# Optimization experiments

Hardware: AMD Instinct MI355X
Metric: run time of the kernel (lower is better)

## Reference

```python
import jax, jax.numpy as jnp
import numpy as np

N = 300000   # number of occupied voxels (sparse tensor rows)
L = 100      # grid side length -> 1e6 cells, occupancy 0.3
C = 32       # channels (channelwise/depthwise conv)
KS = 3       # kernel_size per axis
D = 3        # spatial dimension
R = (KS - 1) // 2


def _build_sparse_structure():
    """Sample N unique voxel coords and build kernel maps (edge lists) like
    MinkowskiEngine's coordinate manager: for each kernel offset, pairs
    (in_idx, out_idx) such that coords[in_idx] == coords[out_idx] + offset."""
    rng = np.random.default_rng(0)
    flat = rng.choice(L ** 3, size=N, replace=False)
    coords = np.stack([flat // (L * L), (flat // L) % L, flat % L], axis=1).astype(np.int32)
    keys = flat.astype(np.int64)
    order = np.argsort(keys)
    sk = keys[order]
    out_ids = np.arange(N, dtype=np.int64)
    in_list, out_list = [], []
    for dx in range(-R, R + 1):
        for dy in range(-R, R + 1):
            for dz in range(-R, R + 1):
                nx = coords[:, 0].astype(np.int64) + dx
                ny = coords[:, 1].astype(np.int64) + dy
                nz = coords[:, 2].astype(np.int64) + dz
                inb = (nx >= 0) & (nx < L) & (ny >= 0) & (ny < L) & (nz >= 0) & (nz < L)
                nk = (nx * L + ny) * L + nz
                pos = np.searchsorted(sk, nk)
                pos_c = np.clip(pos, 0, N - 1)
                ok = inb & (sk[pos_c] == nk)
                in_list.append(order[pos_c[ok]])
                out_list.append(out_ids[ok])
    in_idx = np.concatenate(in_list).astype(np.int32)
    out_idx = np.concatenate(out_list).astype(np.int32)
    return coords, in_idx, out_idx


def setup_inputs() -> dict:
    coords, in_idx, out_idx = _build_sparse_structure()
    key = jax.random.key(0)
    k1, k2 = jax.random.split(key)
    in_feats = jax.random.normal(k1, (N, C), dtype=jnp.float32)
    kernel = jax.random.normal(k2, (KS ** D, C), dtype=jnp.float32)  # depthwise kernel
    return {
        "coords": jnp.asarray(coords),
        "in_idx": jnp.asarray(in_idx),
        "out_idx": jnp.asarray(out_idx),
        "in_feats": in_feats,
        "kernel": kernel,
    }


def reference(coords, in_idx, out_idx, in_feats, kernel):
    # index_array = KS ** flip(arange(D)) -> [9, 3, 1] for KS=3, D=3
    index_pow = jnp.array([KS ** (D - 1 - i) for i in range(D)], dtype=jnp.int32)
    # tensor_stride = 1; kernel_coord = (C_in - C_out)//1 + (KS-1)//2, per edge [E, D]
    kernel_coord = coords[in_idx] - coords[out_idx] + R
    k1d = jnp.sum(index_pow[None, :] * kernel_coord, axis=1)  # [E] in [0, KS**D)
    # gather-multiply-scatter: out_F[out] += in_feats[in] * kernel[k1d]
    out_F = jnp.zeros_like(in_feats).at[out_idx].add(in_feats[in_idx] * kernel[k1d])
    return out_F
```

## Files before the change

### kernel.cpp

```cpp
#include <hip/hip_runtime.h>

#define NCH 32
#define GROUPS 8
#define KVOL 27
#define LG 100
#define LP 102
#define RGN 5
#define NRGN 20
#define NREGIONS (NRGN * NRGN * NRGN)
#define BSIDE 7
#define BVOL 343
#define CELLS 125
#define FSTR 9
#define LSTR 28

__global__ void build_dense(const int* __restrict__ coords,
                            int* __restrict__ dense, int N) {
    int i = blockIdx.x * blockDim.x + threadIdx.x;
    if (i >= N) return;
    int x = coords[3 * i + 0];
    int y = coords[3 * i + 1];
    int z = coords[3 * i + 2];
    dense[((size_t)(x + 1) * LP + (y + 1)) * LP + (z + 1)] = i + 1;
}

__global__ __launch_bounds__(256) void gather_conv_region(
        const int* __restrict__ dense,
        const float4* __restrict__ in_feats4,
        const float4* __restrict__ kernel4,
        float4* __restrict__ out4) {
    __shared__ float4 kw[(KVOL + 1) * FSTR];
    __shared__ int brick[BVOL];
    __shared__ int slotrow[BVOL];
    __shared__ int qcell[CELLS];
    __shared__ int fillA[CELLS];
    __shared__ int smap[CELLS];
    __shared__ int hist[7];
    __shared__ __align__(8) unsigned short list[CELLS * LSTR];
    __shared__ int nslots, nint;

    int tid = threadIdx.x;
    int g   = tid & 7;

    if (tid == 0) { nslots = 0; nint = 0; }
    if (tid < 7) hist[tid] = 0;
    if (tid < CELLS) fillA[tid] = 0;
    if (tid < (KVOL + 1) * GROUPS) {
        int kr = tid >> 3;
        kw[kr * FSTR + g] = (kr < KVOL) ? kernel4[kr * GROUPS + g]
                                        : make_float4(0.f, 0.f, 0.f, 0.f);
    }

    int b = blockIdx.x;
    int r = (b & 7) * (NREGIONS >> 3) + (b >> 3);
    int bx = r / (NRGN * NRGN);
    int by = (r / NRGN) % NRGN;
    int bz = r % NRGN;
    int ox = bx * RGN, oy = by * RGN, oz = bz * RGN;

    for (int i = tid; i < BVOL; i += 256) {
        int lx = i / (BSIDE * BSIDE), ly = (i / BSIDE) % BSIDE, lz = i % BSIDE;
        int v = dense[((size_t)(ox + lx) * LP + (oy + ly)) * LP + (oz + lz)];
        int s = 0;
        if (v > 0) {
            s = atomicAdd(&nslots, 1);
            slotrow[s] = v - 1;
            if ((unsigned)(lx - 1) < RGN && (unsigned)(ly - 1) < RGN &&
                (unsigned)(lz - 1) < RGN) {
                int p = atomicAdd(&nint, 1);
                qcell[p] = (s << 16) | i;
            }
            s += 1;
        }
        brick[i] = s;
    }
    __syncthreads();

    int n = nint;

    for (int idx = tid; idx < n * KVOL; idx += 256) {
        int p = idx / KVOL;
        int k = idx - p * KVOL;
        int cell = qcell[p] & 0xffff;
        int dx = k / 9 - 1, dy = (k / 3) % 3 - 1, dz = k % 3 - 1;
        int nb = brick[cell + dx * (BSIDE * BSIDE) + dy * BSIDE + dz];
        if (nb) {
            int pos = atomicAdd(&fillA[p], 1);
            list[p * LSTR + pos] = (unsigned short)(((nb - 1) << 5) | k);
        }
    }
    __syncthreads();

    if (tid < n) {
        int j = fillA[tid];
        int s = qcell[tid] >> 16;
        unsigned short dummy = (unsigned short)((s << 5) | KVOL);
        while (j & 3) list[tid * LSTR + (j++)] = dummy;
        int bin = (j >> 2) - 1;
        int h = atomicAdd(&hist[bin], 1);
        fillA[tid] = j | (bin << 8) | (h << 16);
    }
    __syncthreads();

    if (tid < n) {
        int f = fillA[tid];
        int j = f & 255, bin = (f >> 8) & 255, h = f >> 16;
        int pos = h;
        for (int bb = bin + 1; bb < 7; ++bb) pos += hist[bb];
        smap[pos] = (tid << 8) | j;
    }
    __syncthreads();

    int lr = tid >> 3;
    for (int base = 0; base < n; base += 32) {
        int lo = base + lr;
        if (lo < n) {
            int d  = smap[lo];
            int p  = d >> 8;
            int nq = (d & 255) >> 2;
            int orow = slotrow[qcell[p] >> 16];
            const uint2* tl2 = (const uint2*)&list[p * LSTR];
            float4 acc = make_float4(0.f, 0.f, 0.f, 0.f);
            for (int jq = 0; jq < nq; ++jq) {
                uint2 L = tl2[jq];
                int e0 = L.x & 0xffff, e1 = L.x >> 16;
                int e2 = L.y & 0xffff, e3 = L.y >> 16;
                int r0 = slotrow[e0 >> 5], r1 = slotrow[e1 >> 5];
                int r2 = slotrow[e2 >> 5], r3 = slotrow[e3 >> 5];
                float4 f0 = in_feats4[(size_t)r0 * GROUPS + g];
                float4 f1 = in_feats4[(size_t)r1 * GROUPS + g];
                float4 f2 = in_feats4[(size_t)r2 * GROUPS + g];
                float4 f3 = in_feats4[(size_t)r3 * GROUPS + g];
                float4 w0 = kw[(e0 & 31) * FSTR + g];
                float4 w1 = kw[(e1 & 31) * FSTR + g];
                float4 w2 = kw[(e2 & 31) * FSTR + g];
                float4 w3 = kw[(e3 & 31) * FSTR + g];
                acc.x += f0.x * w0.x; acc.y += f0.y * w0.y;
                acc.z += f0.z * w0.z; acc.w += f0.w * w0.w;
                acc.x += f1.x * w1.x; acc.y += f1.y * w1.y;
                acc.z += f1.z * w1.z; acc.w += f1.w * w1.w;
                acc.x += f2.x * w2.x; acc.y += f2.y * w2.y;
                acc.z += f2.z * w2.z; acc.w += f2.w * w2.w;
                acc.x += f3.x * w3.x; acc.y += f3.y * w3.y;
                acc.z += f3.z * w3.z; acc.w += f3.w * w3.w;
            }
            out4[(size_t)orow * GROUPS + g] = acc;
        }
    }
}

__global__ void mink_conv_scatter(const int* __restrict__ coords,
                                  const int* __restrict__ in_idx,
                                  const int* __restrict__ out_idx,
                                  const float4* __restrict__ in_feats4,
                                  const float4* __restrict__ kernel4,
                                  float* __restrict__ out,
                                  int E) {
    __shared__ float4 kws[KVOL * GROUPS];
    for (int i = threadIdx.x; i < KVOL * GROUPS; i += blockDim.x)
        kws[i] = kernel4[i];
    __syncthreads();
    int t = blockIdx.x * blockDim.x + threadIdx.x;
    if (t >= E * GROUPS) return;
    int e = t >> 3, g = t & 7;
    int vi = in_idx[e], vo = out_idx[e];
    int c0 = coords[vi * 3 + 0] - coords[vo * 3 + 0] + 1;
    int c1 = coords[vi * 3 + 1] - coords[vo * 3 + 1] + 1;
    int c2 = coords[vi * 3 + 2] - coords[vo * 3 + 2] + 1;
    int k1d = (c0 * 3 + c1) * 3 + c2;
    float4 f = in_feats4[vi * GROUPS + g];
    float4 w = kws[k1d * GROUPS + g];
    float* o = out + vo * NCH + g * 4;
    atomicAdd(o + 0, f.x * w.x);
    atomicAdd(o + 1, f.y * w.y);
    atomicAdd(o + 2, f.z * w.z);
    atomicAdd(o + 3, f.w * w.w);
}

extern "C" void kernel_launch(void* const* d_in, const int* in_sizes, int n_in,
                              void* d_out, int out_size, void* d_ws, size_t ws_size,
                              hipStream_t stream) {
    const int*   coords   = (const int*)d_in[0];
    const int*   in_idx   = (const int*)d_in[1];
    const int*   out_idx  = (const int*)d_in[2];
    const float* in_feats = (const float*)d_in[3];
    const float* kernel   = (const float*)d_in[4];

    const int E     = in_sizes[1];
    const int Nrows = out_size / NCH;

    const size_t dense_bytes = (size_t)LP * LP * LP * sizeof(int);

    if (ws_size >= dense_bytes) {
        int* dense = (int*)d_ws;
        hipMemsetAsync(dense, 0, dense_bytes, stream);

        int block = 256;
        int grid1 = (Nrows + block - 1) / block;
        build_dense<<<grid1, block, 0, stream>>>(coords, dense, Nrows);

        gather_conv_region<<<NREGIONS, 256, 0, stream>>>(
            dense, (const float4*)in_feats, (const float4*)kernel,
            (float4*)d_out);
    } else {
        hipMemsetAsync(d_out, 0, (size_t)out_size * sizeof(float), stream);
        int total = E * GROUPS;
        int block = 256;
        int grid  = (total + block - 1) / block;
        mink_conv_scatter<<<grid, block, 0, stream>>>(
            coords, in_idx, out_idx,
            (const float4*)in_feats, (const float4*)kernel,
            (float*)d_out, E);
    }
}
```

Before: 139.0 us.

## Drop dense-grid memset via coord validation and rebuild neighbor lists with ballots

The dense lookup grid is no longer cleared each call. Each brick cell instead validates its entry by reading the row's coordinates and checking they match the cell, which tolerates stale workspace contents. Neighbor list construction now uses an 8-lane-per-cell ballot/popcount compaction instead of shared atomics. List entries become 32-bit words packing the global row and a byte offset into the shared weights, which removes the slotrow indirection in the inner loop. This trades the memset traffic for an extra coords gather per brick cell and a doubled shared list footprint.

Result: slower. 147.1 us (+5.8%).

```diff
diff --git a/kernel.cpp b/kernel.cpp
--- a/kernel.cpp
+++ b/kernel.cpp
@@ -25,26 +25,26 @@
 }
 
 __global__ __launch_bounds__(256) void gather_conv_region(
+        const int* __restrict__ coords,
         const int* __restrict__ dense,
         const float4* __restrict__ in_feats4,
         const float4* __restrict__ kernel4,
-        float4* __restrict__ out4) {
+        float4* __restrict__ out4, int N) {
     __shared__ float4 kw[(KVOL + 1) * FSTR];
     __shared__ int brick[BVOL];
-    __shared__ int slotrow[BVOL];
     __shared__ int qcell[CELLS];
     __shared__ int fillA[CELLS];
-    __shared__ int smap[CELLS];
+    __shared__ int smapq[CELLS];
+    __shared__ int smapr[CELLS];
     __shared__ int hist[7];
-    __shared__ __align__(8) unsigned short list[CELLS * LSTR];
-    __shared__ int nslots, nint;
+    __shared__ unsigned int list[CELLS * LSTR];
+    __shared__ int nint;
 
     int tid = threadIdx.x;
     int g   = tid & 7;
 
-    if (tid == 0) { nslots = 0; nint = 0; }
+    if (tid == 0) nint = 0;
     if (tid < 7) hist[tid] = 0;
-    if (tid < CELLS) fillA[tid] = 0;
     if (tid < (KVOL + 1) * GROUPS) {
         int kr = tid >> 3;
         kw[kr * FSTR + g] = (kr < KVOL) ? kernel4[kr * GROUPS + g]
@@ -59,82 +59,96 @@
     int ox = bx * RGN, oy = by * RGN, oz = bz * RGN;
 
     for (int i = tid; i < BVOL; i += 256) {
-        int lx = i / (BSIDE * BSIDE), ly = (i / BSIDE) % BSIDE, lz = i % BSIDE;
-        int v = dense[((size_t)(ox + lx) * LP + (oy + ly)) * LP + (oz + lz)];
-        int s = 0;
-        if (v > 0) {
-            s = atomicAdd(&nslots, 1);
-            slotrow[s] = v - 1;
-            if ((unsigned)(lx - 1) < RGN && (unsigned)(ly - 1) < RGN &&
-                (unsigned)(lz - 1) < RGN) {
-                int p = atomicAdd(&nint, 1);
-                qcell[p] = (s << 16) | i;
+        int lx = i / 49, ly = (i / 7) % 7, lz = i % 7;
+        int gx = ox + lx - 1, gy = oy + ly - 1, gz = oz + lz - 1;
+        int v = dense[((size_t)(gx + 1) * LP + (gy + 1)) * LP + (gz + 1)];
+        int row = v - 1;
+        int val = 0;
+        if ((unsigned)row < (unsigned)N) {
+            const int* c = coords + (size_t)row * 3;
+            if (c[0] == gx && c[1] == gy && c[2] == gz) val = v;
+        }
+        brick[i] = val;
+        if (val && (unsigned)(lx - 1) < RGN && (unsigned)(ly - 1) < RGN &&
+            (unsigned)(lz - 1) < RGN) {
+            int p = atomicAdd(&nint, 1);
+            qcell[p] = i;
+        }
+    }
+    __syncthreads();
+
+    int n = nint;
+
+    int oct = tid >> 3, l = tid & 7;
+    int rounds = (n + 31) >> 5;
+    for (int rd = 0; rd < rounds; ++rd) {
+        int q = (rd << 5) + oct;
+        bool valid = q < n;
+        int cell = valid ? qcell[q] : 0;
+        int cnt = 0;
+        unsigned base = (unsigned)q * LSTR;
+        #pragma unroll
+        for (int s = 0; s < 4; ++s) {
+            int k = l + (s << 3);
+            int nb = 0;
+            if (valid && k < KVOL) {
+                int off = (k / 9) * 49 + ((k / 3) % 3) * 7 + (k % 3) - 57;
+                nb = brick[cell + off];
             }
-            s += 1;
-        }
-        brick[i] = s;
-    }
-    __syncthreads();
-
-    int n = nint;
-
-    for (int idx = tid; idx < n * KVOL; idx += 256) {
-        int p = idx / KVOL;
-        int k = idx - p * KVOL;
-        int cell = qcell[p] & 0xffff;
-        int dx = k / 9 - 1, dy = (k / 3) % 3 - 1, dz = k % 3 - 1;
-        int nb = brick[cell + dx * (BSIDE * BSIDE) + dy * BSIDE + dz];
-        if (nb) {
-            int pos = atomicAdd(&fillA[p], 1);
-            list[p * LSTR + pos] = (unsigned short)(((nb - 1) << 5) | k);
-        }
-    }
-    __syncthreads();
-
-    if (tid < n) {
-        int j = fillA[tid];
-        int s = qcell[tid] >> 16;
-        unsigned short dummy = (unsigned short)((s << 5) | KVOL);
-        while (j & 3) list[tid * LSTR + (j++)] = dummy;
-        int bin = (j >> 2) - 1;
-        int h = atomicAdd(&hist[bin], 1);
-        fillA[tid] = j | (bin << 8) | (h << 16);
+            unsigned long long bal = __ballot(nb > 0);
+            int byte = (int)((bal >> ((oct & 7) << 3)) & 0xFF);
+            if (nb > 0) {
+                int pos = cnt + __popc(byte & ((1 << l) - 1));
+                list[base + pos] =
+                    ((unsigned)(nb - 1) << 13) | (unsigned)(k * 144);
+            }
+            cnt += __popc(byte);
+        }
+        if (valid && l == 0) {
+            int j = cnt;
+            unsigned dummy = ((unsigned)(brick[cell] - 1) << 13) | (27u * 144u);
+            while (j & 3) list[base + (j++)] = dummy;
+            int bin = (j >> 2) - 1;
+            int h = atomicAdd(&hist[bin], 1);
+            fillA[q] = (h << 8) | j;
+        }
     }
     __syncthreads();
 
     if (tid < n) {
         int f = fillA[tid];
-        int j = f & 255, bin = (f >> 8) & 255, h = f >> 16;
-        int pos = h;
-        for (int bb = bin + 1; bb < 7; ++bb) pos += hist[bb];
-        smap[pos] = (tid << 8) | j;
-    }
-    __syncthreads();
-
+        int j = f & 255;
+        int bin = (j >> 2) - 1;
+        int pos = f >> 8;
+        #pragma unroll
+        for (int bb = 1; bb < 7; ++bb)
+            if (bb > bin) pos += hist[bb];
+        smapq[pos] = (tid << 8) | j;
+        smapr[pos] = brick[qcell[tid]] - 1;
+    }
+    __syncthreads();
+
+    const char* kwb = (const char*)kw + (g << 4);
     int lr = tid >> 3;
     for (int base = 0; base < n; base += 32) {
         int lo = base + lr;
         if (lo < n) {
-            int d  = smap[lo];
-            int p  = d >> 8;
-            int nq = (d & 255) >> 2;
-            int orow = slotrow[qcell[p] >> 16];
-            const uint2* tl2 = (const uint2*)&list[p * LSTR];
+            int d    = smapq[lo];
+            int q    = d >> 8;
+            int nq   = (d & 255) >> 2;
+            int orow = smapr[lo];
+            const uint4* tl = (const uint4*)&list[(unsigned)q * LSTR];
             float4 acc = make_float4(0.f, 0.f, 0.f, 0.f);
             for (int jq = 0; jq < nq; ++jq) {
-                uint2 L = tl2[jq];
-                int e0 = L.x & 0xffff, e1 = L.x >> 16;
-                int e2 = L.y & 0xffff, e3 = L.y >> 16;
-                int r0 = slotrow[e0 >> 5], r1 = slotrow[e1 >> 5];
-                int r2 = slotrow[e2 >> 5], r3 = slotrow[e3 >> 5];
-                float4 f0 = in_feats4[(size_t)r0 * GROUPS + g];
-                float4 f1 = in_feats4[(size_t)r1 * GROUPS + g];
-                float4 f2 = in_feats4[(size_t)r2 * GROUPS + g];
-                float4 f3 = in_feats4[(size_t)r3 * GROUPS + g];
-                float4 w0 = kw[(e0 & 31) * FSTR + g];
-                float4 w1 = kw[(e1 & 31) * FSTR + g];
-                float4 w2 = kw[(e2 & 31) * FSTR + g];
-                float4 w3 = kw[(e3 & 31) * FSTR + g];
+                uint4 L = tl[jq];
+                float4 f0 = in_feats4[(size_t)(L.x >> 13) * GROUPS + g];
+                float4 f1 = in_feats4[(size_t)(L.y >> 13) * GROUPS + g];
+                float4 f2 = in_feats4[(size_t)(L.z >> 13) * GROUPS + g];
+                float4 f3 = in_feats4[(size_t)(L.w >> 13) * GROUPS + g];
+                float4 w0 = *(const float4*)(kwb + (L.x & 0x1FFFu));
+                float4 w1 = *(const float4*)(kwb + (L.y & 0x1FFFu));
+                float4 w2 = *(const float4*)(kwb + (L.z & 0x1FFFu));
+                float4 w3 = *(const float4*)(kwb + (L.w & 0x1FFFu));
                 acc.x += f0.x * w0.x; acc.y += f0.y * w0.y;
                 acc.z += f0.z * w0.z; acc.w += f0.w * w0.w;
                 acc.x += f1.x * w1.x; acc.y += f1.y * w1.y;
@@ -193,15 +207,13 @@
 
     if (ws_size >= dense_bytes) {
         int* dense = (int*)d_ws;
-        hipMemsetAsync(dense, 0, dense_bytes, stream);
-
         int block = 256;
         int grid1 = (Nrows + block - 1) / block;
         build_dense<<<grid1, block, 0, stream>>>(coords, dense, Nrows);
 
         gather_conv_region<<<NREGIONS, 256, 0, stream>>>(
-            dense, (const float4*)in_feats, (const float4*)kernel,
-            (float4*)d_out);
+            coords, dense, (const float4*)in_feats, (const float4*)kernel,
+            (float4*)d_out, Nrows);
     } else {
         hipMemsetAsync(d_out, 0, (size_t)out_size * sizeof(float), stream);
         int total = E * GROUPS;
```
